# Kernel optimization log

Measured on AMD Instinct MI355X. Metric: run time of the kernel, lower is better.

## Reference

```python
import jax, jax.numpy as jnp
import numpy as np

EPS = 1e-12  # F.normalize default eps

def _unfold3(x):
    # torch F.unfold(kernel=(3,3), padding=1): [B,C,H,W] -> [B, C*9, H*W]
    # channel-major, kernel offsets row-major (matches torch ordering)
    B, C, H, W = x.shape
    xp = jnp.pad(x, ((0, 0), (0, 0), (1, 1), (1, 1)))
    p = jnp.stack([xp[:, :, i:i + H, j:j + W] for i in range(3) for j in range(3)], axis=2)  # [B,C,9,H,W]
    return p.reshape(B, C * 9, H * W)

def _fold3(u, H, W):
    # torch F.fold(output_size=(H,W), kernel=(3,3), padding=1): sums overlapping patches
    B, CK, L = u.shape
    C = CK // 9
    p = u.reshape(B, C, 3, 3, H, W)
    out = jnp.zeros((B, C, H + 2, W + 2), u.dtype)
    for i in range(3):
        for j in range(3):
            out = out.at[:, :, i:i + H, j:j + W].add(p[:, :, i, j])
    return out[:, :, 1:H + 1, 1:W + 1]

def setup_inputs() -> dict:
    key = jax.random.key(0)
    k1, k2, k3 = jax.random.split(key, 3)
    B, C, H, W = 4, 64, 64, 64
    return {
        "lrsr_lv3": jax.random.normal(k1, (B, C, H, W), jnp.float32),
        "refsr_lv3": jax.random.normal(k2, (B, C, H, W), jnp.float32),
        "ref_lv3": jax.random.normal(k3, (B, C, H, W), jnp.float32),
    }

def reference(lrsr_lv3, refsr_lv3, ref_lv3):
    B, C, H, W = lrsr_lv3.shape
    lr_u = _unfold3(lrsr_lv3)                         # [B, D, L_lr], D = C*9
    rs_u = _unfold3(refsr_lv3).transpose(0, 2, 1)     # [B, L_ref, D]
    rs_u = rs_u / jnp.maximum(jnp.linalg.norm(rs_u, axis=2, keepdims=True), EPS)
    lr_u = lr_u / jnp.maximum(jnp.linalg.norm(lr_u, axis=1, keepdims=True), EPS)
    corr = jnp.einsum('brd,bdl->brl', rs_u, lr_u)     # [B, L_ref, L_lr]
    s = jnp.max(corr, axis=1)                         # [B, L_lr]
    arg = jnp.argmax(corr, axis=1)                    # [B, L_lr]
    ref_u = _unfold3(ref_lv3)                         # [B, D, L_ref]
    trans_u = jnp.take_along_axis(ref_u, arg[:, None, :], axis=2)  # [B, D, L_lr]
    trans_lv3 = _fold3(trans_u, H, W)                 # [B, C, H, W]
    return s.reshape(B, 1, H, W), trans_lv3
```

## Files before the change

kernel.cpp:

```cpp
#include <hip/hip_runtime.h>

#define BATCH 4
#define CH    64
#define HH    64
#define WW    64
#define LL    4096
#define SPLITS 4
#define RPS   1024
#define BM    128
#define BN    128

#define RSTRIDE 112

#define WS_SSQ_RS 0
#define WS_SSQ_LR 16384
#define WS_INV_RS 32768
#define WS_INV_LR 49152
#define WS_PMAX   65536
#define WS_PARG   131072
#define WS_ARG    196608

typedef __attribute__((ext_vector_type(8))) short short8b;
typedef __attribute__((ext_vector_type(4))) short short4b;
typedef __attribute__((ext_vector_type(4))) float f32x4;

__global__ void k_ssq(const float* __restrict__ lrsr,
                      const float* __restrict__ refsr,
                      float* __restrict__ ws) {
    int t = blockIdx.x * 256 + threadIdx.x;
    int b = t >> 12;
    int r = t & (LL - 1);
    const float* pl = lrsr + (size_t)b * CH * LL + r;
    const float* pr = refsr + (size_t)b * CH * LL + r;
    float sl = 0.f, sr = 0.f;
    #pragma unroll 8
    for (int c = 0; c < CH; ++c) {
        float a = pl[c * LL]; sl += a * a;
        float d = pr[c * LL]; sr += d * d;
    }
    ws[WS_SSQ_RS + t] = sr;
    ws[WS_SSQ_LR + t] = sl;
}

__global__ void k_inv(float* __restrict__ ws) {
    int t = blockIdx.x * 256 + threadIdx.x;
    int b = t >> 12;
    int r = t & (LL - 1);
    int y = r >> 6, x = r & 63;
    float srs = 0.f, slr = 0.f;
    for (int di = -1; di <= 1; ++di) {
        int yy = y + di;
        if ((unsigned)yy >= (unsigned)HH) continue;
        for (int dj = -1; dj <= 1; ++dj) {
            int xx = x + dj;
            if ((unsigned)xx >= (unsigned)WW) continue;
            int idx = b * LL + yy * WW + xx;
            srs += ws[WS_SSQ_RS + idx];
            slr += ws[WS_SSQ_LR + idx];
        }
    }
    ws[WS_INV_RS + t] = 1.f / fmaxf(sqrtf(srs), 1e-12f);
    ws[WS_INV_LR + t] = 1.f / fmaxf(sqrtf(slr), 1e-12f);
}

__global__ __launch_bounds__(256, 2)
void k_corrmax(const float* __restrict__ lrsr,
               const float* __restrict__ refsr,
               float* __restrict__ ws) {
    __shared__ __align__(16) unsigned short As[BM * RSTRIDE];
    __shared__ __align__(16) unsigned short Bs[BN * RSTRIDE];

    int tid  = threadIdx.x;
    int b    = blockIdx.z;
    int l0   = blockIdx.x * BN;
    int rbs  = blockIdx.y * RPS;

    const float* xr = refsr + (size_t)b * CH * LL;
    const float* xl = lrsr  + (size_t)b * CH * LL;
    const float* invn_rs = ws + WS_INV_RS + b * LL;

    int lane = tid & 63;
    int wid  = tid >> 6;
    int wr   = wid >> 1;
    int wc   = wid & 1;
    int ln   = lane & 15;
    int g    = lane >> 4;

    int p  = tid & 63;
    int kp = tid >> 6;

    int abase[4], bbase[4];
    #pragma unroll
    for (int mf = 0; mf < 4; ++mf) {
        int rloc = wr * 64 + mf * 16 + ln;
        abase[mf] = rloc * RSTRIDE + ((g ^ ((rloc >> 2) & 3)) << 3);
        int lloc = wc * 64 + mf * 16 + ln;
        bbase[mf] = lloc * RSTRIDE + ((g ^ ((lloc >> 2) & 3)) << 3);
    }

    float run_m = -1e30f;
    int   run_a = 0;

    for (int rt = 0; rt < RPS / BM; ++rt) {
        int r0 = rbs + rt * BM;

        f32x4 acc[4][4];
        #pragma unroll
        for (int mf = 0; mf < 4; ++mf)
            #pragma unroll
            for (int nf = 0; nf < 4; ++nf)
                acc[mf][nf] = (f32x4){0.f, 0.f, 0.f, 0.f};

        for (int q = 0; q < 9; ++q) {
            int i = q / 3 - 1;
            int j = q % 3 - 1;
            int off = i * WW + j;
            bool okA[2], okB[2];
            const float* gA[2];
            const float* gB[2];
            #pragma unroll
            for (int rh = 0; rh < 2; ++rh) {
                int pp = p + rh * 64;
                int rpos = r0 + pp;
                okA[rh] = ((unsigned)((rpos >> 6) + i) < (unsigned)HH) &&
                          ((unsigned)((rpos & 63) + j) < (unsigned)WW);
                gA[rh] = xr + (okA[rh] ? rpos + off : 0) + kp * 8 * LL;
                int lpos = l0 + pp;
                okB[rh] = ((unsigned)((lpos >> 6) + i) < (unsigned)HH) &&
                          ((unsigned)((lpos & 63) + j) < (unsigned)WW);
                gB[rh] = xl + (okB[rh] ? lpos + off : 0) + kp * 8 * LL;
            }

            for (int h = 0; h < 2; ++h) {
                int choff = h * 32 * LL;
                __syncthreads();
                #pragma unroll
                for (int rh = 0; rh < 2; ++rh) {
                    int pp = p + rh * 64;
                    int rowbase = pp * RSTRIDE + ((kp ^ ((pp >> 2) & 3)) << 3);
                    #pragma unroll
                    for (int side = 0; side < 2; ++side) {
                        const float* gp = (side ? gB[rh] : gA[rh]) + choff;
                        bool ok = side ? okB[rh] : okA[rh];
                        unsigned short* S = side ? Bs : As;
                        #pragma unroll
                        for (int i4 = 0; i4 < 2; ++i4) {
                            float v[4];
                            #pragma unroll
                            for (int c4 = 0; c4 < 4; ++c4)
                                v[c4] = gp[(i4 * 4 + c4) * LL];
                            short4b w0, w1, w2;
                            #pragma unroll
                            for (int c4 = 0; c4 < 4; ++c4) {
                                float x = ok ? v[c4] : 0.f;
                                unsigned u0 = __float_as_uint(x);
                                float f0 = __uint_as_float(u0 & 0xffff0000u);
                                float r1 = x - f0;
                                unsigned u1 = __float_as_uint(r1);
                                float f1 = __uint_as_float(u1 & 0xffff0000u);
                                float r2 = r1 - f1;
                                w0[c4] = (short)(u0 >> 16);
                                w1[c4] = (short)(u1 >> 16);
                                w2[c4] = (short)(__float_as_uint(r2) >> 16);
                            }
                            int idx = rowbase + i4 * 4;
                            *(short4b*)&S[idx]          = w0;
                            *(short4b*)&S[idx + 32]     = w1;
                            *(short4b*)&S[idx + 64]     = w2;
                        }
                    }
                }
                __syncthreads();
                short8b a[4][3], bb[4][3];
                #pragma unroll
                for (int mf = 0; mf < 4; ++mf)
                    #pragma unroll
                    for (int c = 0; c < 3; ++c) {
                        a[mf][c]  = *(const short8b*)&As[abase[mf] + c * 32];
                        bb[mf][c] = *(const short8b*)&Bs[bbase[mf] + c * 32];
                    }
                #pragma unroll
                for (int mf = 0; mf < 4; ++mf)
                    #pragma unroll
                    for (int nf = 0; nf < 4; ++nf) {
                        f32x4 d = acc[mf][nf];
                        d = __builtin_amdgcn_mfma_f32_16x16x32_bf16(a[mf][0], bb[nf][0], d, 0, 0, 0);
                        d = __builtin_amdgcn_mfma_f32_16x16x32_bf16(a[mf][0], bb[nf][1], d, 0, 0, 0);
                        d = __builtin_amdgcn_mfma_f32_16x16x32_bf16(a[mf][1], bb[nf][0], d, 0, 0, 0);
                        d = __builtin_amdgcn_mfma_f32_16x16x32_bf16(a[mf][1], bb[nf][1], d, 0, 0, 0);
                        d = __builtin_amdgcn_mfma_f32_16x16x32_bf16(a[mf][0], bb[nf][2], d, 0, 0, 0);
                        d = __builtin_amdgcn_mfma_f32_16x16x32_bf16(a[mf][2], bb[nf][0], d, 0, 0, 0);
                        acc[mf][nf] = d;
                    }
            }
        }

        __syncthreads();
        float* sm = (float*)As;
        int*   si = (int*)((float*)As + 256);
        #pragma unroll
        for (int nf = 0; nf < 4; ++nf) {
            float bv = -1e30f; int bi = 0;
            #pragma unroll
            for (int mf = 0; mf < 4; ++mf) {
                #pragma unroll
                for (int reg = 0; reg < 4; ++reg) {
                    int r = r0 + wr * 64 + mf * 16 + g * 4 + reg;
                    float val = acc[mf][nf][reg] * invn_rs[r];
                    if (val > bv || (val == bv && r < bi)) { bv = val; bi = r; }
                }
            }
            #pragma unroll
            for (int ofs = 16; ofs < 64; ofs <<= 1) {
                float ov = __shfl_xor(bv, ofs);
                int   oi = __shfl_xor(bi, ofs);
                if (ov > bv || (ov == bv && oi < bi)) { bv = ov; bi = oi; }
            }
            if (g == 0) {
                int col = wc * 64 + nf * 16 + ln;
                sm[wr * 128 + col] = bv;
                si[wr * 128 + col] = bi;
            }
        }
        __syncthreads();
        if (tid < 128) {
            float bm = run_m; int ba = run_a;
            #pragma unroll
            for (int w = 0; w < 2; ++w) {
                float v = sm[w * 128 + tid];
                int   a2 = si[w * 128 + tid];
                if (v > bm || (v == bm && a2 < ba)) { bm = v; ba = a2; }
            }
            run_m = bm; run_a = ba;
        }
    }

    if (tid < 128) {
        int l = l0 + tid;
        int o = (b * SPLITS + blockIdx.y) * LL + l;
        ws[WS_PMAX + o] = run_m;
        ((int*)ws)[WS_PARG + o] = run_a;
    }
}

__global__ void k_reduce(float* __restrict__ ws, float* __restrict__ out) {
    int t = blockIdx.x * 256 + threadIdx.x;
    int b = t >> 12;
    int l = t & (LL - 1);
    float bm = -1e30f; int ba = 0;
    for (int s = 0; s < SPLITS; ++s) {
        int o = (b * SPLITS + s) * LL + l;
        float v = ws[WS_PMAX + o];
        int   a = ((int*)ws)[WS_PARG + o];
        if (v > bm || (v == bm && a < ba)) { bm = v; ba = a; }
    }
    out[t] = bm * ws[WS_INV_LR + t];
    ((int*)ws)[WS_ARG + t] = ba;
}

__global__ void k_fold(const float* __restrict__ ref,
                       const float* __restrict__ ws,
                       float* __restrict__ out) {
    int t = blockIdx.x * 256 + threadIdx.x;
    int b = t >> 18;
    int c = (t >> 12) & 63;
    int yx = t & (LL - 1);
    int y = yx >> 6, x = yx & 63;
    const int* ab = ((const int*)ws) + WS_ARG + b * LL;
    const float* rb = ref + (size_t)b * CH * LL + c * LL;
    float s = 0.f;
    #pragma unroll
    for (int i = 0; i < 3; ++i) {
        int yp = y + 1 - i;
        if ((unsigned)yp >= (unsigned)HH) continue;
        #pragma unroll
        for (int j = 0; j < 3; ++j) {
            int xp = x + 1 - j;
            if ((unsigned)xp >= (unsigned)WW) continue;
            int r = ab[yp * WW + xp];
            int ry = (r >> 6) + i - 1;
            int rx = (r & 63) + j - 1;
            if ((unsigned)ry < (unsigned)HH && (unsigned)rx < (unsigned)WW)
                s += rb[ry * WW + rx];
        }
    }
    out[BATCH * LL + t] = s;
}

extern "C" void kernel_launch(void* const* d_in, const int* in_sizes, int n_in,
                              void* d_out, int out_size, void* d_ws, size_t ws_size,
                              hipStream_t stream) {
    const float* lrsr = (const float*)d_in[0];
    const float* refsr = (const float*)d_in[1];
    const float* ref  = (const float*)d_in[2];
    float* out = (float*)d_out;
    float* ws  = (float*)d_ws;

    k_ssq<<<dim3(BATCH * LL / 256), dim3(256), 0, stream>>>(lrsr, refsr, ws);
    k_inv<<<dim3(BATCH * LL / 256), dim3(256), 0, stream>>>(ws);
    k_corrmax<<<dim3(LL / BN, SPLITS, BATCH), dim3(256), 0, stream>>>(lrsr, refsr, ws);
    k_reduce<<<dim3(BATCH * LL / 256), dim3(256), 0, stream>>>(ws, out);
    k_fold<<<dim3(BATCH * CH * LL / 256), dim3(256), 0, stream>>>(ref, ws, out);
}
```

Baseline: 464.2 us.

## Pre-split inputs into padded bf16x3 buffer and stream tiles via async LDS loads

A new pre-pass converts both inputs once into a zero-padded, channel-grouped bf16 three-way split layout in workspace, so the correlation kernel no longer redoes the split and bounds checks for every tap. The main kernel then fills shared memory with direct global-to-LDS loads and issues the next tile's loads before the current MFMA block, overlapping memory with compute. This adds a memset plus an extra pass over inputs, a larger workspace, and relies on the padded layout and swizzle being correct.

```diff
diff --git a/kernel.cpp b/kernel.cpp
--- a/kernel.cpp
+++ b/kernel.cpp
@@ -9,8 +9,17 @@
 #define RPS   1024
 #define BM    128
 #define BN    128
-
-#define RSTRIDE 112
+#define NRT   (RPS/BM)
+
+#define RSTB  192
+#define BSOFF 24576
+
+#define PAD_L   4356
+#define GP_BYTE_BASE 1048576
+#define GP_SIDE_STRIDE 6690816
+#define GP_B_STRIDE    1672704
+#define GP_COMP_STRIDE 557568
+#define GP_TOTAL       13381632
 
 #define WS_SSQ_RS 0
 #define WS_SSQ_LR 16384
@@ -21,8 +30,44 @@
 #define WS_ARG    196608
 
 typedef __attribute__((ext_vector_type(8))) short short8b;
-typedef __attribute__((ext_vector_type(4))) short short4b;
 typedef __attribute__((ext_vector_type(4))) float f32x4;
+
+__device__ __forceinline__ void gload16(const void* g, void* l) {
+    __builtin_amdgcn_global_load_lds(
+        (const __attribute__((address_space(1))) unsigned int*)g,
+        (__attribute__((address_space(3))) unsigned int*)l, 16, 0, 0);
+}
+
+__global__ void k_split(const float* __restrict__ lrsr,
+                        const float* __restrict__ refsr,
+                        float* __restrict__ ws) {
+    int tid  = threadIdx.x;
+    int pos  = blockIdx.x * 256 + tid;
+    int c8   = blockIdx.y;
+    int side = blockIdx.z >> 2;
+    int b    = blockIdx.z & 3;
+    const float* src = (side ? lrsr : refsr) + (size_t)b * CH * LL + c8 * 8 * LL + pos;
+    int ppos = (pos >> 6) * 66 + (pos & 63) + 67;
+    char* dst = (char*)ws + GP_BYTE_BASE + side * GP_SIDE_STRIDE + b * GP_B_STRIDE
+              + (size_t)(c8 * PAD_L + ppos) * 16;
+    union { unsigned short u[8]; uint4 v; } w0, w1, w2;
+    #pragma unroll
+    for (int cc = 0; cc < 8; ++cc) {
+        float x = src[cc * LL];
+        unsigned u0 = __float_as_uint(x);
+        float f0 = __uint_as_float(u0 & 0xffff0000u);
+        float r1 = x - f0;
+        unsigned u1 = __float_as_uint(r1);
+        float f1 = __uint_as_float(u1 & 0xffff0000u);
+        float r2 = r1 - f1;
+        w0.u[cc] = (unsigned short)(u0 >> 16);
+        w1.u[cc] = (unsigned short)(u1 >> 16);
+        w2.u[cc] = (unsigned short)(__float_as_uint(r2) >> 16);
+    }
+    *(uint4*)(dst)                      = w0.v;
+    *(uint4*)(dst + GP_COMP_STRIDE)     = w1.v;
+    *(uint4*)(dst + 2 * GP_COMP_STRIDE) = w2.v;
+}
 
 __global__ void k_ssq(const float* __restrict__ lrsr,
                       const float* __restrict__ refsr,
@@ -64,44 +109,73 @@
 }
 
 __global__ __launch_bounds__(256, 2)
-void k_corrmax(const float* __restrict__ lrsr,
-               const float* __restrict__ refsr,
-               float* __restrict__ ws) {
-    __shared__ __align__(16) unsigned short As[BM * RSTRIDE];
-    __shared__ __align__(16) unsigned short Bs[BN * RSTRIDE];
+void k_corrmax(float* __restrict__ ws) {
+    __shared__ __align__(16) unsigned short LDSB[24576];
+    __shared__ float sm[256];
+    __shared__ int   si[256];
 
     int tid  = threadIdx.x;
     int b    = blockIdx.z;
     int l0   = blockIdx.x * BN;
     int rbs  = blockIdx.y * RPS;
 
-    const float* xr = refsr + (size_t)b * CH * LL;
-    const float* xl = lrsr  + (size_t)b * CH * LL;
-    const float* invn_rs = ws + WS_INV_RS + b * LL;
-
     int lane = tid & 63;
-    int wid  = tid >> 6;
-    int wr   = wid >> 1;
-    int wc   = wid & 1;
+    int w    = tid >> 6;
+    int wr   = w >> 1;
+    int wc   = w & 1;
     int ln   = lane & 15;
     int g    = lane >> 4;
 
-    int p  = tid & 63;
-    int kp = tid >> 6;
-
-    int abase[4], bbase[4];
+    const float* invn_rs = ws + WS_INV_RS + b * LL;
+    const char* gp  = (const char*)ws + GP_BYTE_BASE + b * GP_B_STRIDE;
+    const char* bp  = gp + ((w < 2) ? 0 : GP_SIDE_STRIDE);
+
+    int LC[12];
+    int LB[12];
+    {
+        int wm = (w & 1) * 12;
+        #pragma unroll
+        for (int n = 0; n < 12; ++n) {
+            int mm  = wm + n;
+            int G   = mm * 64 + lane;
+            int row = G / 12;
+            int rem = G - row * 12;
+            int comp = rem >> 2;
+            int sl   = rem & 3;
+            int o    = sl ^ ((row >> 2) & 3);
+            LC[n] = (comp * (8 * PAD_L) + o * PAD_L + row + 2 * (row >> 6)) * 16;
+            LB[n] = ((w < 2) ? 0 : BSOFF) + mm * 1024;
+        }
+    }
+
+    int arow[4], brow[4];
+    int swz = (g ^ ((ln >> 2) & 3)) << 4;
     #pragma unroll
     for (int mf = 0; mf < 4; ++mf) {
-        int rloc = wr * 64 + mf * 16 + ln;
-        abase[mf] = rloc * RSTRIDE + ((g ^ ((rloc >> 2) & 3)) << 3);
-        int lloc = wc * 64 + mf * 16 + ln;
-        bbase[mf] = lloc * RSTRIDE + ((g ^ ((lloc >> 2) & 3)) << 3);
-    }
+        arow[mf] = (wr * 64 + mf * 16 + ln) * RSTB + swz;
+        brow[mf] = BSOFF + (wc * 64 + mf * 16 + ln) * RSTB + swz;
+    }
+
+    int y0B = l0 >> 6;
+    int y0A0 = rbs >> 6;
+
+    auto issue = [&](int rt2, int q2, int h2) {
+        int i2 = (q2 < 3) ? -1 : ((q2 < 6) ? 0 : 1);
+        int j2 = q2 - (i2 + 1) * 3 - 1;
+        int y0 = (w < 2) ? (y0A0 + rt2 * 2) : y0B;
+        int su = (h2 * (4 * PAD_L) + (y0 + 1 + i2) * 66 + 1 + j2) * 16;
+        #pragma unroll
+        for (int n = 0; n < 12; ++n)
+            gload16(bp + (su + LC[n]), (char*)LDSB + LB[n]);
+    };
 
     float run_m = -1e30f;
     int   run_a = 0;
 
-    for (int rt = 0; rt < RPS / BM; ++rt) {
+    issue(0, 0, 0);
+    __syncthreads();
+
+    for (int rt = 0; rt < NRT; ++rt) {
         int r0 = rbs + rt * BM;
 
         f32x4 acc[4][4];
@@ -112,73 +186,24 @@
                 acc[mf][nf] = (f32x4){0.f, 0.f, 0.f, 0.f};
 
         for (int q = 0; q < 9; ++q) {
-            int i = q / 3 - 1;
-            int j = q % 3 - 1;
-            int off = i * WW + j;
-            bool okA[2], okB[2];
-            const float* gA[2];
-            const float* gB[2];
-            #pragma unroll
-            for (int rh = 0; rh < 2; ++rh) {
-                int pp = p + rh * 64;
-                int rpos = r0 + pp;
-                okA[rh] = ((unsigned)((rpos >> 6) + i) < (unsigned)HH) &&
-                          ((unsigned)((rpos & 63) + j) < (unsigned)WW);
-                gA[rh] = xr + (okA[rh] ? rpos + off : 0) + kp * 8 * LL;
-                int lpos = l0 + pp;
-                okB[rh] = ((unsigned)((lpos >> 6) + i) < (unsigned)HH) &&
-                          ((unsigned)((lpos & 63) + j) < (unsigned)WW);
-                gB[rh] = xl + (okB[rh] ? lpos + off : 0) + kp * 8 * LL;
-            }
-
             for (int h = 0; h < 2; ++h) {
-                int choff = h * 32 * LL;
-                __syncthreads();
-                #pragma unroll
-                for (int rh = 0; rh < 2; ++rh) {
-                    int pp = p + rh * 64;
-                    int rowbase = pp * RSTRIDE + ((kp ^ ((pp >> 2) & 3)) << 3);
-                    #pragma unroll
-                    for (int side = 0; side < 2; ++side) {
-                        const float* gp = (side ? gB[rh] : gA[rh]) + choff;
-                        bool ok = side ? okB[rh] : okA[rh];
-                        unsigned short* S = side ? Bs : As;
-                        #pragma unroll
-                        for (int i4 = 0; i4 < 2; ++i4) {
-                            float v[4];
-                            #pragma unroll
-                            for (int c4 = 0; c4 < 4; ++c4)
-                                v[c4] = gp[(i4 * 4 + c4) * LL];
-                            short4b w0, w1, w2;
-                            #pragma unroll
-                            for (int c4 = 0; c4 < 4; ++c4) {
-                                float x = ok ? v[c4] : 0.f;
-                                unsigned u0 = __float_as_uint(x);
-                                float f0 = __uint_as_float(u0 & 0xffff0000u);
-                                float r1 = x - f0;
-                                unsigned u1 = __float_as_uint(r1);
-                                float f1 = __uint_as_float(u1 & 0xffff0000u);
-                                float r2 = r1 - f1;
-                                w0[c4] = (short)(u0 >> 16);
-                                w1[c4] = (short)(u1 >> 16);
-                                w2[c4] = (short)(__float_as_uint(r2) >> 16);
-                            }
-                            int idx = rowbase + i4 * 4;
-                            *(short4b*)&S[idx]          = w0;
-                            *(short4b*)&S[idx + 32]     = w1;
-                            *(short4b*)&S[idx + 64]     = w2;
-                        }
-                    }
-                }
-                __syncthreads();
                 short8b a[4][3], bb[4][3];
+                const char* lc = (const char*)LDSB;
                 #pragma unroll
                 for (int mf = 0; mf < 4; ++mf)
                     #pragma unroll
                     for (int c = 0; c < 3; ++c) {
-                        a[mf][c]  = *(const short8b*)&As[abase[mf] + c * 32];
-                        bb[mf][c] = *(const short8b*)&Bs[bbase[mf] + c * 32];
+                        a[mf][c]  = *(const short8b*)(lc + arow[mf] + c * 64);
+                        bb[mf][c] = *(const short8b*)(lc + brow[mf] + c * 64);
                     }
+                __syncthreads();
+
+                {
+                    int h2 = h ^ 1, q2 = q, rt2 = rt;
+                    if (h == 1) { q2 = q + 1; h2 = 0; if (q2 == 9) { q2 = 0; rt2 = rt + 1; } }
+                    issue(rt2, q2, h2);
+                }
+
                 #pragma unroll
                 for (int mf = 0; mf < 4; ++mf)
                     #pragma unroll
@@ -192,12 +217,10 @@
                         d = __builtin_amdgcn_mfma_f32_16x16x32_bf16(a[mf][2], bb[nf][0], d, 0, 0, 0);
                         acc[mf][nf] = d;
                     }
-            }
-        }
-
-        __syncthreads();
-        float* sm = (float*)As;
-        int*   si = (int*)((float*)As + 256);
+                __syncthreads();
+            }
+        }
+
         #pragma unroll
         for (int nf = 0; nf < 4; ++nf) {
             float bv = -1e30f; int bi = 0;
@@ -226,13 +249,14 @@
         if (tid < 128) {
             float bm = run_m; int ba = run_a;
             #pragma unroll
-            for (int w = 0; w < 2; ++w) {
-                float v = sm[w * 128 + tid];
-                int   a2 = si[w * 128 + tid];
+            for (int ww = 0; ww < 2; ++ww) {
+                float v = sm[ww * 128 + tid];
+                int   a2 = si[ww * 128 + tid];
                 if (v > bm || (v == bm && a2 < ba)) { bm = v; ba = a2; }
             }
             run_m = bm; run_a = ba;
         }
+        __syncthreads();
     }
 
     if (tid < 128) {
@@ -296,9 +320,11 @@
     float* out = (float*)d_out;
     float* ws  = (float*)d_ws;
 
+    hipMemsetAsync((char*)d_ws + GP_BYTE_BASE, 0, GP_TOTAL, stream);
+    k_split<<<dim3(16, 8, 8), dim3(256), 0, stream>>>(lrsr, refsr, ws);
     k_ssq<<<dim3(BATCH * LL / 256), dim3(256), 0, stream>>>(lrsr, refsr, ws);
     k_inv<<<dim3(BATCH * LL / 256), dim3(256), 0, stream>>>(ws);
-    k_corrmax<<<dim3(LL / BN, SPLITS, BATCH), dim3(256), 0, stream>>>(lrsr, refsr, ws);
+    k_corrmax<<<dim3(LL / BN, SPLITS, BATCH), dim3(256), 0, stream>>>(ws);
     k_reduce<<<dim3(BATCH * LL / 256), dim3(256), 0, stream>>>(ws, out);
     k_fold<<<dim3(BATCH * CH * LL / 256), dim3(256), 0, stream>>>(ref, ws, out);
 }
```

After: 425.9 us. 8.3% less time.
